# Kernel tuning notes

Hardware: AMD Instinct MI355X
Metric: run time of the kernel (lower is better)

Reference implementation:

```python
import jax, jax.numpy as jnp
import numpy as np

B, N, D, H, HD = 4, 2048, 512, 8, 64
FF = 1024
C2, HF, WF = 128, 64, 64
EPS = 1e-6


def setup_inputs() -> dict:
    key = jax.random.key(0)
    ks = jax.random.split(key, 9)
    def nrm(k, shape, s=0.02):
        return jax.random.normal(k, shape, dtype=jnp.float32) * s
    x = jax.random.normal(ks[0], (B, N, D), dtype=jnp.float32)
    theta = jax.random.normal(ks[1], (B, H, N, HD // 2), dtype=jnp.float32)
    fmaps = jax.random.normal(ks[2], (B, C2, HF, WF), dtype=jnp.float32)
    # pixel-unit (x, y) coords in [0, W-1] / [0, H-1]
    coords = jax.random.uniform(ks[3], (B, N, 2), dtype=jnp.float32) * (WF - 1)
    return dict(
        x=x, theta=theta, fmaps=fmaps, coords=coords,
        w_corr=nrm(ks[4], (D, C2)),
        norm1_scale=jnp.ones((D,), jnp.float32),
        qk_scale_q=jnp.ones((HD,), jnp.float32),
        qk_scale_k=jnp.ones((HD,), jnp.float32),
        w_qkv=nrm(ks[5], (3 * D, D)),
        w_out=nrm(ks[6], (D, D)),
        norm2_scale=jnp.ones((D,), jnp.float32),
        w_ff1=nrm(ks[7], (2 * FF, D)),
        b_ff1=jnp.zeros((2 * FF,), jnp.float32),
        w_ff2=nrm(ks[8], (D, FF)),
    )


def rms_norm(x, scale, eps=EPS):
    ms = jnp.mean(jnp.square(x), axis=-1, keepdims=True)
    return x * (scale * jax.lax.rsqrt(ms + eps))


def apply_rotary(x, theta):
    # rotates first 2*d channels of the head dim, as in _apply_rotary_emb_inplace
    d = theta.shape[-1]
    x1, x2 = x[..., :d], x[..., d:2 * d]
    cos, sin = jnp.cos(theta), jnp.sin(theta)
    y1 = x1 * cos - x2 * sin
    y2 = x2 * cos + x1 * sin
    return jnp.concatenate([y1, y2, x[..., 2 * d:]], axis=-1)


def bilinear_sample(fmaps, coords):
    # fmaps [B,C,H,W], coords [B,N,2] (x,y) pixels; border padding, align_corners=True
    Hh, Ww = fmaps.shape[-2], fmaps.shape[-1]
    xc = jnp.clip(coords[..., 0], 0.0, Ww - 1.0)
    yc = jnp.clip(coords[..., 1], 0.0, Hh - 1.0)
    x0 = jnp.floor(xc); y0 = jnp.floor(yc)
    wx = xc - x0; wy = yc - y0
    x0i = x0.astype(jnp.int32); x1i = jnp.minimum(x0i + 1, Ww - 1)
    y0i = y0.astype(jnp.int32); y1i = jnp.minimum(y0i + 1, Hh - 1)
    def gather_one(img, yi, xi):  # img [C,H,W] -> [C,N]
        return img[:, yi, xi]
    g = jax.vmap(gather_one)
    f00 = g(fmaps, y0i, x0i); f01 = g(fmaps, y0i, x1i)
    f10 = g(fmaps, y1i, x0i); f11 = g(fmaps, y1i, x1i)
    wx = wx[:, None, :]; wy = wy[:, None, :]
    top = f00 * (1.0 - wx) + f01 * wx
    bot = f10 * (1.0 - wx) + f11 * wx
    out = top * (1.0 - wy) + bot * wy  # [B,C,N]
    return jnp.transpose(out, (0, 2, 1))  # [B,N,C]


def reference(x, theta, fmaps, coords, w_corr, norm1_scale, qk_scale_q,
              qk_scale_k, w_qkv, w_out, norm2_scale, w_ff1, b_ff1, w_ff2):
    # correlation features injected into tokens
    feats = bilinear_sample(fmaps, coords)          # [B,N,C2]
    x = x + feats @ w_corr.T                        # [B,N,D]
    # --- attention block (pre-RMSNorm, qk-norm, RoPE, unscaled dot-product attn) ---
    skip = x
    xn = rms_norm(x, norm1_scale)
    qkv = xn @ w_qkv.T                              # [B,N,3D]
    q, k, v = jnp.split(qkv, 3, axis=-1)
    def to_heads(t):
        return jnp.transpose(t.reshape(t.shape[0], t.shape[1], H, HD), (0, 2, 1, 3))
    q, k, v = to_heads(q), to_heads(k), to_heads(v)  # [B,H,N,HD]
    q = rms_norm(q, qk_scale_q)
    k = rms_norm(k, qk_scale_k)
    q = apply_rotary(q, theta)
    k = apply_rotary(k, theta)
    # dot_product_attn: raw q @ k^T (no 1/sqrt(d)), softmax, @ v
    attn = jax.nn.softmax(jnp.einsum('bhid,bhjd->bhij', q, k), axis=-1)
    o = jnp.einsum('bhij,bhjd->bhid', attn, v)
    o = jnp.transpose(o, (0, 2, 1, 3)).reshape(x.shape[0], x.shape[1], D)
    x = skip + o @ w_out.T
    # --- feedforward block (GEGLU) ---
    skip = x
    xn = rms_norm(x, norm2_scale)
    h = xn @ w_ff1.T + b_ff1
    hx, gate = jnp.split(h, 2, axis=-1)
    h = hx * jax.nn.gelu(gate, approximate=False)
    return skip + h @ w_ff2.T
```

## Files before the change

### kernel.cpp

```cpp
#include <hip/hip_runtime.h>
#include <hip/hip_bf16.h>
#include <math.h>

#define Bsz 4
#define Nseq 2048
#define Dm 512
#define Hn 8
#define HDm 64
#define FFm 1024
#define Cc 128
#define EPSf 1e-6f

typedef __attribute__((ext_vector_type(8))) short short8;
typedef __attribute__((ext_vector_type(4))) float f32x4;
typedef __attribute__((ext_vector_type(16))) float f32x16;
typedef __attribute__((ext_vector_type(4))) unsigned u32x4;

#define AS1(p) ((__attribute__((address_space(1))) void*)((void*)(p)))
#define AS3(p) ((__attribute__((address_space(3))) void*)(p))

__device__ __forceinline__ float bf2f(unsigned short u) {
    return __uint_as_float(((unsigned)u) << 16);
}
__device__ __forceinline__ unsigned short f2bf(float f) {
    unsigned u = __float_as_uint(f);
    return (unsigned short)((u + 0x7fffu + ((u >> 16) & 1u)) >> 16);
}
__device__ __forceinline__ unsigned cvt_pk_bf16(float lo, float hi) {
    unsigned r;
    asm("v_cvt_pk_bf16_f32 %0, %1, %2" : "=v"(r) : "v"(lo), "v"(hi));
    return r;
}
__device__ __forceinline__ bool is_f32(const unsigned* dtp) {
    return dtp[0] == 0x3F800000u;
}

#define LOG2E 1.4426950408889634f
#define SHIFT2 92.33248261689366f

#define CONV_TOTAL 2690176
__global__ __launch_bounds__(256) void convert_kernel(
    const void* s0, const void* s1, const void* s2, const void* s3,
    const void* s4, const void* s5, const void* s6, const void* s7,
    const void* s8, const void* s9,
    unsigned short* __restrict__ canon, const unsigned* __restrict__ dtp)
{
    int i = blockIdx.x * 256 + threadIdx.x;
    if (i >= CONV_TOTAL) return;
    const void* src; int j;
    if      (i < 786432)  { src = s0; j = i; }
    else if (i < 1835008) {
        src = s1;
        int j0 = i - 786432;
        int rr = j0 >> 9, cc = j0 & 511;
        int q = rr >> 4, tt = rr & 15;
        j = ((q & 1) * 1024 + (q >> 1) * 16 + tt) * 512 + cc;
    }
    else if (i < 2359296) { src = s2; j = i - 1835008; }
    else if (i < 2621440) { src = s3; j = i - 2359296; }
    else if (i < 2686976) { src = s4; j = i - 2621440; }
    else if (i < 2689024) {
        src = s5;
        int j0 = i - 2686976;
        int q = j0 >> 4, tt = j0 & 15;
        j = (q & 1) * 1024 + (q >> 1) * 16 + tt;
    }
    else if (i < 2689536) { src = s6; j = i - 2689024; }
    else if (i < 2690048) { src = s7; j = i - 2689536; }
    else if (i < 2690112) { src = s8; j = i - 2690048; }
    else                  { src = s9; j = i - 2690112; }
    canon[i] = is_f32(dtp) ? f2bf(((const float*)src)[j])
                           : ((const unsigned short*)src)[j];
}

__global__ __launch_bounds__(256) void sample_kernel(
    const void* __restrict__ fmaps,
    const void* __restrict__ coords,
    unsigned short* __restrict__ feats,
    const unsigned* __restrict__ dtp)
{
    const bool f32m = is_f32(dtp);
    int i = blockIdx.x * 256 + threadIdx.x;
    int t = i >> 7;
    int c = i & 127;
    int b = t >> 11;
    float xc, yc;
    if (f32m) { xc = ((const float*)coords)[2 * t];  yc = ((const float*)coords)[2 * t + 1]; }
    else      { xc = bf2f(((const unsigned short*)coords)[2 * t]);
                yc = bf2f(((const unsigned short*)coords)[2 * t + 1]); }
    xc = fminf(fmaxf(xc, 0.f), 63.f);
    yc = fminf(fmaxf(yc, 0.f), 63.f);
    float x0f = floorf(xc), y0f = floorf(yc);
    float wx = xc - x0f, wy = yc - y0f;
    int x0 = (int)x0f, y0 = (int)y0f;
    int x1 = min(x0 + 1, 63), y1 = min(y0 + 1, 63);
    size_t fb = ((size_t)b * Cc + c) << 12;
    float f00, f01, f10, f11;
    if (f32m) {
        const float* fp = (const float*)fmaps + fb;
        f00 = fp[(y0 << 6) + x0]; f01 = fp[(y0 << 6) + x1];
        f10 = fp[(y1 << 6) + x0]; f11 = fp[(y1 << 6) + x1];
    } else {
        const unsigned short* fp = (const unsigned short*)fmaps + fb;
        f00 = bf2f(fp[(y0 << 6) + x0]); f01 = bf2f(fp[(y0 << 6) + x1]);
        f10 = bf2f(fp[(y1 << 6) + x0]); f11 = bf2f(fp[(y1 << 6) + x1]);
    }
    float top = f00 * (1.f - wx) + f01 * wx;
    float bot = f10 * (1.f - wx) + f11 * wx;
    feats[i] = f2bf(top * (1.f - wy) + bot * wy);
}

template<int BN>
__global__ __launch_bounds__(256, 4) void gemm_bt(
    const unsigned short* __restrict__ A,
    const unsigned short* __restrict__ W,
    const unsigned short* __restrict__ bias,
    const float* __restrict__ resF,
    const void* __restrict__ resRaw,
    float* __restrict__ outF,
    unsigned short* __restrict__ outB,
    void* __restrict__ outRaw,
    unsigned short* __restrict__ outG,
    const unsigned* __restrict__ dtp,
    int M, int N, int K)
{
    constexpr int NT = BN / 32;
    __shared__ __align__(16) unsigned short As[2][128 * 32];
    __shared__ __align__(16) unsigned short Bs[2][BN * 32];
    const int tid = threadIdx.x;
    const int wave = tid >> 6, lane = tid & 63;
    const int quad = lane >> 4, l16 = lane & 15;
    const int wm = wave >> 1, wn = wave & 1;
    const int rowBase = blockIdx.y * 128;
    const int colBase = blockIdx.x * BN;
    const unsigned short* Ab = A + (size_t)rowBase * K;
    const unsigned short* Wb = W + (size_t)colBase * K;
    const int sr = lane >> 2;
    const int sc = (lane & 3) * 8;

    f32x4 acc[4][NT] = {};

    auto stage = [&](int buf, int k0) {
#pragma unroll
        for (int c = 0; c < 2; ++c) {
            int chunk = wave + c * 4;
            const unsigned short* ga = Ab + (size_t)(chunk * 16 + sr) * K + k0 + sc;
            __builtin_amdgcn_global_load_lds(AS1(ga), AS3(&As[buf][chunk * 512]), 16, 0, 0);
        }
#pragma unroll
        for (int c = 0; c < BN / 16; c += 4) {
            int chunk = wave + c;
            const unsigned short* gb = Wb + (size_t)(chunk * 16 + sr) * K + k0 + sc;
            __builtin_amdgcn_global_load_lds(AS1(gb), AS3(&Bs[buf][chunk * 512]), 16, 0, 0);
        }
    };

    const int nk = K >> 5;
    stage(0, 0);
    for (int kt = 0; kt < nk; ++kt) {
        const int buf = kt & 1;
        __syncthreads();
        __builtin_amdgcn_sched_barrier(0);
        if (kt + 1 < nk) stage(1 - buf, (kt + 1) << 5);
        short8 af[4], bfr[NT];
#pragma unroll
        for (int mt = 0; mt < 4; ++mt)
            af[mt] = *(const short8*)&As[buf][(wm * 64 + mt * 16 + l16) * 32 + quad * 8];
#pragma unroll
        for (int nt = 0; nt < NT; ++nt)
            bfr[nt] = *(const short8*)&Bs[buf][(wn * (BN / 2) + nt * 16 + l16) * 32 + quad * 8];
        __builtin_amdgcn_s_setprio(1);
#pragma unroll
        for (int mt = 0; mt < 4; ++mt)
#pragma unroll
            for (int nt = 0; nt < NT; ++nt)
                acc[mt][nt] = __builtin_amdgcn_mfma_f32_16x16x32_bf16(
                    af[mt], bfr[nt], acc[mt][nt], 0, 0, 0);
        __builtin_amdgcn_s_setprio(0);
    }

    if (outG) {
#pragma unroll
        for (int mt = 0; mt < 4; ++mt)
#pragma unroll
            for (int r = 0; r < 4; ++r) {
                int row = rowBase + wm * 64 + mt * 16 + quad * 4 + r;
#pragma unroll
                for (int nt = 0; nt < NT; nt += 2) {
                    int colh = colBase + wn * (BN / 2) + nt * 16 + l16;
                    float hx = acc[mt][nt][r]     + bf2f(bias[colh]);
                    float g  = acc[mt][nt + 1][r] + bf2f(bias[colh + 16]);
                    float gl = 0.5f * g * (1.f + erff(g * 0.70710678118654752f));
                    int pc = (colBase >> 1) + wn * (BN / 4) + (nt >> 1) * 16 + l16;
                    outG[(size_t)row * FFm + pc] = f2bf(hx * gl);
                }
            }
        return;
    }
    const bool f32m = dtp ? is_f32(dtp) : false;
#pragma unroll
    for (int mt = 0; mt < 4; ++mt) {
#pragma unroll
        for (int r = 0; r < 4; ++r) {
            int row = rowBase + wm * 64 + mt * 16 + quad * 4 + r;
            size_t rowoff = (size_t)row * N;
#pragma unroll
            for (int nt = 0; nt < NT; ++nt) {
                int col = colBase + wn * (BN / 2) + nt * 16 + l16;
                float v = acc[mt][nt][r];
                if (bias) v += bf2f(bias[col]);
                size_t idx = rowoff + col;
                if (resF) v += resF[idx];
                if (resRaw) v += f32m ? ((const float*)resRaw)[idx]
                                      : bf2f(((const unsigned short*)resRaw)[idx]);
                if (outF)      outF[idx] = v;
                else if (outB) outB[idx] = f2bf(v);
                else if (f32m) ((float*)outRaw)[idx] = v;
                else           ((unsigned short*)outRaw)[idx] = f2bf(v);
            }
        }
    }
}

__global__ __launch_bounds__(256) void rmsnorm_kernel(
    const float* __restrict__ X, const unsigned short* __restrict__ scale,
    unsigned short* __restrict__ Y)
{
    int t = blockIdx.x;
    int tid = threadIdx.x;
    const float* xr = X + (size_t)t * 512;
    float a = xr[tid], b = xr[tid + 256];
    float ss = a * a + b * b;
#pragma unroll
    for (int off = 1; off < 64; off <<= 1) ss += __shfl_xor(ss, off);
    __shared__ float red[4];
    int wave = tid >> 6, lane = tid & 63;
    if (lane == 0) red[wave] = ss;
    __syncthreads();
    float tot = red[0] + red[1] + red[2] + red[3];
    float r = rsqrtf(tot * (1.f / 512.f) + EPSf);
    Y[(size_t)t * 512 + tid]       = f2bf(a * (bf2f(scale[tid]) * r));
    Y[(size_t)t * 512 + tid + 256] = f2bf(b * (bf2f(scale[tid + 256]) * r));
}

__global__ __launch_bounds__(256) void qkv_rope_kernel(
    const unsigned short* __restrict__ qkv, const void* __restrict__ theta,
    const unsigned short* __restrict__ sq, const unsigned short* __restrict__ sk,
    unsigned short* __restrict__ Qo, unsigned short* __restrict__ Ko,
    const unsigned* __restrict__ dtp)
{
    const bool f32m = is_f32(dtp);
    int t = blockIdx.x;
    int b = t >> 11, n = t & 2047;
    int wave = threadIdx.x >> 6, lane = threadIdx.x & 63;
    const unsigned short* base = qkv + (size_t)t * 1536;
#pragma unroll
    for (int hh = 0; hh < 2; ++hh) {
        int h = wave + hh * 4;
        float q = bf2f(base[h * 64 + lane]);
        float k = bf2f(base[512 + h * 64 + lane]);
        float ssq = q * q, ssk = k * k;
#pragma unroll
        for (int off = 1; off < 64; off <<= 1) {
            ssq += __shfl_xor(ssq, off);
            ssk += __shfl_xor(ssk, off);
        }
        float qn = q * (bf2f(sq[lane]) * rsqrtf(ssq * (1.f / 64.f) + EPSf));
        float kn = k * (bf2f(sk[lane]) * rsqrtf(ssk * (1.f / 64.f) + EPSf));
        size_t thIdx = ((size_t)(b * Hn + h) * Nseq + n) * 32 + (lane & 31);
        float th = f32m ? ((const float*)theta)[thIdx]
                        : bf2f(((const unsigned short*)theta)[thIdx]);
        float cth = __cosf(th), sth = __sinf(th);
        float qp = __shfl_xor(qn, 32);
        float kp = __shfl_xor(kn, 32);
        float sgn = (lane < 32) ? -1.f : 1.f;
        float qr = qn * cth + sgn * qp * sth;
        float kr = kn * cth + sgn * kp * sth;
        size_t o = ((size_t)(b * Hn + h) * Nseq + n) * 64 + lane;
        Qo[o] = f2bf(qr * LOG2E);
        Ko[o] = f2bf(kr);
    }
}

__global__ __launch_bounds__(256) void vtrans_kernel(
    const unsigned short* __restrict__ qkvb, unsigned short* __restrict__ Vt)
{
    int bh = blockIdx.y;
    int b = bh >> 3, h = bh & 7;
    int tid = threadIdx.x;
    int d = tid & 63;
    int chunk = blockIdx.x * 4 + (tid >> 6);
    int n0 = chunk * 8;
    unsigned short v[8];
#pragma unroll
    for (int j = 0; j < 8; ++j)
        v[j] = qkvb[((size_t)(b * Nseq + n0 + j)) * 1536 + 1024 + h * 64 + d];
    *(short8*)&Vt[((size_t)bh * 64 + d) * Nseq + n0] = *(short8*)v;
}

__global__ __launch_bounds__(256, 4) void attn_kernel(
    const unsigned short* __restrict__ Qg,
    const unsigned short* __restrict__ Kg,
    const unsigned short* __restrict__ Vtg,
    float* __restrict__ Op,
    float* __restrict__ Lp)
{
    const int bh = blockIdx.x;
    const int b = bh >> 3, h = bh & 7;
    const int q0 = blockIdx.y * 128;
    const int kz = blockIdx.z;
    const int tid = threadIdx.x;
    const int wave = tid >> 6, lane = tid & 63;
    const int l31 = lane & 31, hh = lane >> 5;
    __shared__ __align__(16) unsigned short Ks[2][64 * 72];
    __shared__ __align__(16) unsigned short Vs[2][64 * 72];
    const size_t bhN = (size_t)bh * Nseq;

    short8 bq[4];
#pragma unroll
    for (int kc = 0; kc < 4; ++kc)
        bq[kc] = *(const short8*)&Qg[(bhN + q0 + wave * 32 + l31) * 64 + kc * 16 + hh * 8];

    f32x16 oa[2] = {};
    float lsum = 0.f;
    const int r8 = tid >> 3;
    const int c8e = (tid & 7) * 8;
    const unsigned short* kgb = Kg + bhN * 64;
    const unsigned short* vbase = Vtg + (size_t)bh * 64 * Nseq;
    const bool hi = (hh == 1);

    const int KT0 = kz * (Nseq / 128);
    const int KT1 = KT0 + (Nseq / 128);
    const int kb0 = KT0 * 64;

    short8 kr0 = *(const short8*)&kgb[(size_t)(kb0 + r8) * 64 + c8e];
    short8 kr1 = *(const short8*)&kgb[(size_t)(kb0 + r8 + 32) * 64 + c8e];
    short8 vr0 = *(const short8*)&vbase[(size_t)r8 * Nseq + kb0 + c8e];
    short8 vr1 = *(const short8*)&vbase[(size_t)(r8 + 32) * Nseq + kb0 + c8e];

    for (int kt = KT0; kt < KT1; ++kt) {
        const int cur = kt & 1;
        *(short8*)&Ks[cur][r8 * 72 + c8e]        = kr0;
        *(short8*)&Ks[cur][(r8 + 32) * 72 + c8e] = kr1;
        *(short8*)&Vs[cur][r8 * 72 + c8e]        = vr0;
        *(short8*)&Vs[cur][(r8 + 32) * 72 + c8e] = vr1;
        __syncthreads();
        __builtin_amdgcn_sched_barrier(0);
        if (kt + 1 < KT1) {
            const int kb = (kt + 1) * 64;
            kr0 = *(const short8*)&kgb[(size_t)(kb + r8) * 64 + c8e];
            kr1 = *(const short8*)&kgb[(size_t)(kb + r8 + 32) * 64 + c8e];
            vr0 = *(const short8*)&vbase[(size_t)r8 * Nseq + kb + c8e];
            vr1 = *(const short8*)&vbase[(size_t)(r8 + 32) * Nseq + kb + c8e];
        }

        f32x16 st[2];
#pragma unroll
        for (int mt = 0; mt < 2; ++mt)
#pragma unroll
            for (int e = 0; e < 16; ++e) st[mt][e] = -SHIFT2;
        __builtin_amdgcn_s_setprio(1);
#pragma unroll
        for (int kc = 0; kc < 4; ++kc) {
            short8 ak0 = *(const short8*)&Ks[cur][(l31) * 72 + kc * 16 + hh * 8];
            short8 ak1 = *(const short8*)&Ks[cur][(32 + l31) * 72 + kc * 16 + hh * 8];
            st[0] = __builtin_amdgcn_mfma_f32_32x32x16_bf16(ak0, bq[kc], st[0], 0, 0, 0);
            st[1] = __builtin_amdgcn_mfma_f32_32x32x16_bf16(ak1, bq[kc], st[1], 0, 0, 0);
        }
        __builtin_amdgcn_s_setprio(0);

        unsigned pk[2][8];
        float partial = 0.f;
#pragma unroll
        for (int t = 0; t < 2; ++t)
#pragma unroll
            for (int p = 0; p < 4; ++p) {
                float v0 = __builtin_amdgcn_exp2f(st[t][4 * p + 0]);
                float v1 = __builtin_amdgcn_exp2f(st[t][4 * p + 1]);
                float v2 = __builtin_amdgcn_exp2f(st[t][4 * p + 2]);
                float v3 = __builtin_amdgcn_exp2f(st[t][4 * p + 3]);
                partial += (v0 + v1) + (v2 + v3);
                pk[t][2 * p + 0] = cvt_pk_bf16(v0, v1);
                pk[t][2 * p + 1] = cvt_pk_bf16(v2, v3);
            }
        lsum += partial + __shfl_xor(partial, 32);

        __builtin_amdgcn_s_setprio(1);
#pragma unroll
        for (int kc = 0; kc < 4; ++kc) {
            const int tau = kc >> 1;
            const int pA = 2 * (kc & 1);
            const int pB = pA + 1;
            unsigned dA0 = pk[tau][2 * pA], dA1 = pk[tau][2 * pA + 1];
            unsigned dB0 = pk[tau][2 * pB], dB1 = pk[tau][2 * pB + 1];
            unsigned s0 = hi ? dA0 : dB0, s1 = hi ? dA1 : dB1;
            unsigned r0 = __shfl_xor(s0, 32), r1 = __shfl_xor(s1, 32);
            unsigned o0 = hi ? dB0 : dA0, o1 = hi ? dB1 : dA1;
            u32x4 av = { hi ? r0 : o0, hi ? r1 : o1,
                         hi ? o0 : r0, hi ? o1 : r1 };
            short8 ap = __builtin_bit_cast(short8, av);
            short8 bv0 = *(const short8*)&Vs[cur][(l31) * 72 + kc * 16 + hh * 8];
            short8 bv1 = *(const short8*)&Vs[cur][(32 + l31) * 72 + kc * 16 + hh * 8];
            oa[0] = __builtin_amdgcn_mfma_f32_32x32x16_bf16(ap, bv0, oa[0], 0, 0, 0);
            oa[1] = __builtin_amdgcn_mfma_f32_32x32x16_bf16(ap, bv1, oa[1], 0, 0, 0);
        }
        __builtin_amdgcn_s_setprio(0);
    }

    if (!hi)
        Lp[((size_t)kz * 32 + bh) * Nseq + q0 + wave * 32 + l31] = lsum;
    const size_t obase = (size_t)kz * (Bsz * Nseq);
#pragma unroll
    for (int nt = 0; nt < 2; ++nt)
#pragma unroll
        for (int i = 0; i < 16; ++i) {
            int qr = q0 + wave * 32 + (i & 3) + 8 * (i >> 2) + 4 * hh;
            Op[(obase + (size_t)b * Nseq + qr) * Dm + h * 64 + nt * 32 + l31] =
                oa[nt][i];
        }
}

__global__ __launch_bounds__(256) void attn_combine_kernel(
    const float* __restrict__ Op,
    const float* __restrict__ Lp,
    unsigned short* __restrict__ Og)
{
    int gid = blockIdx.x * 256 + threadIdx.x;
    size_t base = (size_t)gid * 8;
    int t = gid >> 6;
    int c = (gid & 63) * 8;
    int h = c >> 6;
    int bh = ((t >> 11) << 3) + h;
    int n = t & 2047;
    float l = Lp[(size_t)bh * Nseq + n] + Lp[(size_t)(32 * Nseq) + (size_t)bh * Nseq + n];
    float inv = 1.f / l;
    f32x4 a0 = *(const f32x4*)&Op[base];
    f32x4 a1 = *(const f32x4*)&Op[base + 4];
    f32x4 b0 = *(const f32x4*)&Op[(size_t)8192 * 512 + base];
    f32x4 b1 = *(const f32x4*)&Op[(size_t)8192 * 512 + base + 4];
    unsigned short o[8];
#pragma unroll
    for (int j = 0; j < 4; ++j) {
        o[j]     = f2bf((a0[j] + b0[j]) * inv);
        o[4 + j] = f2bf((a1[j] + b1[j]) * inv);
    }
    *(short8*)&Og[base] = *(short8*)o;
}

extern "C" void kernel_launch(void* const* d_in, const int* in_sizes, int n_in,
                              void* d_out, int out_size, void* d_ws, size_t ws_size,
                              hipStream_t stream) {
    const void* x      = d_in[0];
    const void* theta  = d_in[1];
    const void* fmaps  = d_in[2];
    const void* coords = d_in[3];
    const void* w_corr = d_in[4];
    const void* n1s    = d_in[5];
    const void* sq     = d_in[6];
    const void* sk     = d_in[7];
    const void* w_qkv  = d_in[8];
    const void* w_out  = d_in[9];
    const void* n2s    = d_in[10];
    const void* w_ff1  = d_in[11];
    const void* b_ff1  = d_in[12];
    const void* w_ff2  = d_in[13];
    const unsigned* dtp = (const unsigned*)n1s;

    char* ws = (char*)d_ws;
    float*          x1    = (float*)(ws + 0);
    float*          x2    = (float*)(ws + 16777216);
    unsigned short* xn    = (unsigned short*)(ws + 33554432);
    unsigned short* qkvb  = (unsigned short*)(ws + 41943040);
    unsigned short* feats = (unsigned short*)(ws + 41943040);
    unsigned short* qb    = (unsigned short*)(ws + 67108864);
    unsigned short* kb    = (unsigned short*)(ws + 75497472);
    unsigned short* vt    = (unsigned short*)(ws + 83886080);
    unsigned short* ob    = (unsigned short*)(ws + 92274688);
    unsigned short* hbuf  = (unsigned short*)(ws + 75497472);
    unsigned short* canon = (unsigned short*)(ws + 100663296);
    float*          opart = (float*)(ws + 16777216);
    float*          lpart = (float*)(ws + 50331648);
    unsigned short* wqkvc  = canon + 0;
    unsigned short* wff1c  = canon + 786432;
    unsigned short* wff2c  = canon + 1835008;
    unsigned short* woutc  = canon + 2359296;
    unsigned short* wcorrc = canon + 2621440;
    unsigned short* bff1c  = canon + 2686976;
    unsigned short* n1c    = canon + 2689024;
    unsigned short* n2c    = canon + 2689536;
    unsigned short* sqc    = canon + 2690048;
    unsigned short* skc    = canon + 2690112;

    convert_kernel<<<(CONV_TOTAL + 255) / 256, 256, 0, stream>>>(
        w_qkv, w_ff1, w_ff2, w_out, w_corr, b_ff1, n1s, n2s, sq, sk, canon, dtp);
    sample_kernel<<<4096, 256, 0, stream>>>(fmaps, coords, feats, dtp);
    gemm_bt<64><<<dim3(8, 64), 256, 0, stream>>>(feats, wcorrc, nullptr, nullptr, x,
                                                 x1, nullptr, nullptr, nullptr, dtp, 8192, 512, 128);
    rmsnorm_kernel<<<8192, 256, 0, stream>>>(x1, n1c, xn);
    gemm_bt<128><<<dim3(12, 64), 256, 0, stream>>>(xn, wqkvc, nullptr, nullptr, nullptr,
                                                   nullptr, qkvb, nullptr, nullptr, nullptr, 8192, 1536, 512);
    qkv_rope_kernel<<<8192, 256, 0, stream>>>(qkvb, theta, sqc, skc, qb, kb, dtp);
    vtrans_kernel<<<dim3(64, 32), 256, 0, stream>>>(qkvb, vt);
    attn_kernel<<<dim3(32, 16, 2), 256, 0, stream>>>(qb, kb, vt, opart, lpart);
    attn_combine_kernel<<<2048, 256, 0, stream>>>(opart, lpart, ob);
    gemm_bt<64><<<dim3(8, 64), 256, 0, stream>>>(ob, woutc, nullptr, x1, nullptr,
                                                 x2, nullptr, nullptr, nullptr, nullptr, 8192, 512, 512);
    rmsnorm_kernel<<<8192, 256, 0, stream>>>(x2, n2c, xn);
    gemm_bt<128><<<dim3(16, 64), 256, 0, stream>>>(xn, wff1c, bff1c, nullptr, nullptr,
                                                   nullptr, nullptr, nullptr, hbuf, nullptr, 8192, 2048, 512);
    gemm_bt<64><<<dim3(8, 64), 256, 0, stream>>>(hbuf, wff2c, nullptr, x2, nullptr,
                                                 nullptr, nullptr, d_out, nullptr, dtp, 8192, 512, 1024);
}
```

Baseline: 338.0 us.

## Pre-swizzle K and V into MFMA fragment layout and drop LDS staging

The rotary kernel now writes K, and the V-transpose kernel writes V, directly in a per-lane MFMA operand layout (tile, k-chunk, row-half, lane, 8 elements). The attention kernel then loads each lane's fragments with coalesced 16-byte global loads, so the shared-memory double buffer and the per-tile __syncthreads are gone. This removes LDS traffic and the block barrier. In exchange, each of the 4 waves fetches the same K/V tile from global/L2 separately, and the software prefetch into the next iteration is dropped, which can expose memory latency.

```diff
diff --git a/kernel.cpp b/kernel.cpp
--- a/kernel.cpp
+++ b/kernel.cpp
@@ -278,7 +278,11 @@
         float kr = kn * cth + sgn * kp * sth;
         size_t o = ((size_t)(b * Hn + h) * Nseq + n) * 64 + lane;
         Qo[o] = f2bf(qr * LOG2E);
-        Ko[o] = f2bf(kr);
+        int ktn = n >> 6, rhn = (n >> 5) & 1, l31n = n & 31;
+        int kcd = lane >> 4, hhd = (lane >> 3) & 1, jd = lane & 7;
+        size_t koff = (((((size_t)(b * Hn + h) * 32 + ktn) * 4 + kcd) * 2 + rhn) * 64
+                       + hhd * 32 + l31n) * 8 + jd;
+        Ko[koff] = f2bf(kr);
     }
 }
 
@@ -295,13 +299,17 @@
 #pragma unroll
     for (int j = 0; j < 8; ++j)
         v[j] = qkvb[((size_t)(b * Nseq + n0 + j)) * 1536 + 1024 + h * 64 + d];
-    *(short8*)&Vt[((size_t)bh * 64 + d) * Nseq + n0] = *(short8*)v;
+    int ktn = n0 >> 6, kcn = (n0 >> 4) & 3, hhn = (n0 >> 3) & 1;
+    int rhd = d >> 5, l31d = d & 31;
+    size_t voff = (((((size_t)bh * 32 + ktn) * 4 + kcn) * 2 + rhd) * 64
+                   + hhn * 32 + l31d) * 8;
+    *(short8*)&Vt[voff] = *(short8*)v;
 }
 
 __global__ __launch_bounds__(256, 4) void attn_kernel(
     const unsigned short* __restrict__ Qg,
-    const unsigned short* __restrict__ Kg,
-    const unsigned short* __restrict__ Vtg,
+    const unsigned short* __restrict__ Kf,
+    const unsigned short* __restrict__ Vf,
     float* __restrict__ Op,
     float* __restrict__ Lp)
 {
@@ -312,9 +320,8 @@
     const int tid = threadIdx.x;
     const int wave = tid >> 6, lane = tid & 63;
     const int l31 = lane & 31, hh = lane >> 5;
-    __shared__ __align__(16) unsigned short Ks[2][64 * 72];
-    __shared__ __align__(16) unsigned short Vs[2][64 * 72];
     const size_t bhN = (size_t)bh * Nseq;
+    const bool hi = (hh == 1);
 
     short8 bq[4];
 #pragma unroll
@@ -323,35 +330,22 @@
 
     f32x16 oa[2] = {};
     float lsum = 0.f;
-    const int r8 = tid >> 3;
-    const int c8e = (tid & 7) * 8;
-    const unsigned short* kgb = Kg + bhN * 64;
-    const unsigned short* vbase = Vtg + (size_t)bh * 64 * Nseq;
-    const bool hi = (hh == 1);
+
+    const unsigned short* kfb = Kf + (size_t)bh * (32 * 4096) + (size_t)lane * 8;
+    const unsigned short* vfb = Vf + (size_t)bh * (32 * 4096) + (size_t)lane * 8;
 
     const int KT0 = kz * (Nseq / 128);
     const int KT1 = KT0 + (Nseq / 128);
-    const int kb0 = KT0 * 64;
-
-    short8 kr0 = *(const short8*)&kgb[(size_t)(kb0 + r8) * 64 + c8e];
-    short8 kr1 = *(const short8*)&kgb[(size_t)(kb0 + r8 + 32) * 64 + c8e];
-    short8 vr0 = *(const short8*)&vbase[(size_t)r8 * Nseq + kb0 + c8e];
-    short8 vr1 = *(const short8*)&vbase[(size_t)(r8 + 32) * Nseq + kb0 + c8e];
 
     for (int kt = KT0; kt < KT1; ++kt) {
-        const int cur = kt & 1;
-        *(short8*)&Ks[cur][r8 * 72 + c8e]        = kr0;
-        *(short8*)&Ks[cur][(r8 + 32) * 72 + c8e] = kr1;
-        *(short8*)&Vs[cur][r8 * 72 + c8e]        = vr0;
-        *(short8*)&Vs[cur][(r8 + 32) * 72 + c8e] = vr1;
-        __syncthreads();
-        __builtin_amdgcn_sched_barrier(0);
-        if (kt + 1 < KT1) {
-            const int kb = (kt + 1) * 64;
-            kr0 = *(const short8*)&kgb[(size_t)(kb + r8) * 64 + c8e];
-            kr1 = *(const short8*)&kgb[(size_t)(kb + r8 + 32) * 64 + c8e];
-            vr0 = *(const short8*)&vbase[(size_t)r8 * Nseq + kb + c8e];
-            vr1 = *(const short8*)&vbase[(size_t)(r8 + 32) * Nseq + kb + c8e];
+        const unsigned short* kp = kfb + (size_t)kt * 4096;
+        const unsigned short* vp = vfb + (size_t)kt * 4096;
+
+        short8 kf0[4], kf1[4];
+#pragma unroll
+        for (int kc = 0; kc < 4; ++kc) {
+            kf0[kc] = *(const short8*)(kp + kc * 1024);
+            kf1[kc] = *(const short8*)(kp + kc * 1024 + 512);
         }
 
         f32x16 st[2];
@@ -362,12 +356,18 @@
         __builtin_amdgcn_s_setprio(1);
 #pragma unroll
         for (int kc = 0; kc < 4; ++kc) {
-            short8 ak0 = *(const short8*)&Ks[cur][(l31) * 72 + kc * 16 + hh * 8];
-            short8 ak1 = *(const short8*)&Ks[cur][(32 + l31) * 72 + kc * 16 + hh * 8];
-            st[0] = __builtin_amdgcn_mfma_f32_32x32x16_bf16(ak0, bq[kc], st[0], 0, 0, 0);
-            st[1] = __builtin_amdgcn_mfma_f32_32x32x16_bf16(ak1, bq[kc], st[1], 0, 0, 0);
+            st[0] = __builtin_amdgcn_mfma_f32_32x32x16_bf16(kf0[kc], bq[kc], st[0], 0, 0, 0);
+            st[1] = __builtin_amdgcn_mfma_f32_32x32x16_bf16(kf1[kc], bq[kc], st[1], 0, 0, 0);
         }
         __builtin_amdgcn_s_setprio(0);
+        __builtin_amdgcn_sched_barrier(0);
+
+        short8 vf0[4], vf1[4];
+#pragma unroll
+        for (int kc = 0; kc < 4; ++kc) {
+            vf0[kc] = *(const short8*)(vp + kc * 1024);
+            vf1[kc] = *(const short8*)(vp + kc * 1024 + 512);
+        }
 
         unsigned pk[2][8];
         float partial = 0.f;
@@ -399,10 +399,8 @@
             u32x4 av = { hi ? r0 : o0, hi ? r1 : o1,
                          hi ? o0 : r0, hi ? o1 : r1 };
             short8 ap = __builtin_bit_cast(short8, av);
-            short8 bv0 = *(const short8*)&Vs[cur][(l31) * 72 + kc * 16 + hh * 8];
-            short8 bv1 = *(const short8*)&Vs[cur][(32 + l31) * 72 + kc * 16 + hh * 8];
-            oa[0] = __builtin_amdgcn_mfma_f32_32x32x16_bf16(ap, bv0, oa[0], 0, 0, 0);
-            oa[1] = __builtin_amdgcn_mfma_f32_32x32x16_bf16(ap, bv1, oa[1], 0, 0, 0);
+            oa[0] = __builtin_amdgcn_mfma_f32_32x32x16_bf16(ap, vf0[kc], oa[0], 0, 0, 0);
+            oa[1] = __builtin_amdgcn_mfma_f32_32x32x16_bf16(ap, vf1[kc], oa[1], 0, 0, 0);
         }
         __builtin_amdgcn_s_setprio(0);
     }
```

Result: slower. 385.9 us (+14.2%).
